# Kernel tuning notes

Measured on AMD Instinct MI355X. Metric: run time of the kernel, lower is better.

The kernel has to match this reference:

```python
import jax, jax.numpy as jnp
import numpy as np

H, O, E, V = 128, 128, 512, 34
B, T, L = 64, 2048, 256


def _lstm(x, wih, whh, bih, bhh):
    # x: [T, B, Din] -> outputs [T, B, H]; PyTorch gate order i, f, g, o
    n = whh.shape[1]
    h0 = jnp.zeros((x.shape[1], n), x.dtype)
    b = bih + bhh
    def step(carry, xt):
        h, c = carry
        g = xt @ wih.T + h @ whh.T + b
        i, f, gg, o = jnp.split(g, 4, axis=-1)
        c = jax.nn.sigmoid(f) * c + jax.nn.sigmoid(i) * jnp.tanh(gg)
        h = jax.nn.sigmoid(o) * jnp.tanh(c)
        return (h, c), h
    _, ys = jax.lax.scan(step, (h0, h0), x)
    return ys


def _conv1d_s2(x, w, b):
    # x: [B, Cin, T], w: [Cout, Cin, 2], kernel=2 stride=2 valid
    y = jax.lax.conv_general_dilated(x, w, (2,), 'VALID', dimension_numbers=('NCH', 'OIH', 'NCH'))
    return y + b[None, :, None]


def setup_inputs():
    key = jax.random.key(0)
    ctr = [0]
    def mk(shape, s=0.05):
        ctr[0] += 1
        return jax.random.normal(jax.random.fold_in(key, ctr[0]), shape, dtype=jnp.float32) * s
    inp = {}
    inp['utter'] = mk((B, T, 40), 1.0)
    inp['targets'] = jax.random.randint(jax.random.fold_in(key, 999), (B, L), 0, V)
    inp['wih_f'] = mk((4 * H, 40)); inp['whh_f'] = mk((4 * H, H)); inp['bih_f'] = mk((4 * H,)); inp['bhh_f'] = mk((4 * H,))
    inp['wih_r'] = mk((4 * H, 40)); inp['whh_r'] = mk((4 * H, H)); inp['bih_r'] = mk((4 * H,)); inp['bhh_r'] = mk((4 * H,))
    inp['c1w'] = mk((H, 2 * H, 2)); inp['c1b'] = mk((H,))
    inp['wih1'] = mk((4 * H, H)); inp['whh1'] = mk((4 * H, H)); inp['bih1'] = mk((4 * H,)); inp['bhh1'] = mk((4 * H,))
    inp['c2w'] = mk((H, H, 2)); inp['c2b'] = mk((H,))
    inp['wih2'] = mk((4 * H, H)); inp['whh2'] = mk((4 * H, H)); inp['bih2'] = mk((4 * H,)); inp['bhh2'] = mk((4 * H,))
    inp['kw'] = mk((O, H)); inp['kb'] = mk((O,)); inp['vw'] = mk((O, H)); inp['vb'] = mk((O,))
    inp['wihd'] = mk((4 * O, O + E)); inp['whhd'] = mk((4 * O, O)); inp['bihd'] = mk((4 * O,)); inp['bhhd'] = mk((4 * O,))
    inp['w1'] = mk((V, O)); inp['b1'] = mk((V,)); inp['w2'] = mk((V, O)); inp['b2'] = mk((V,))
    inp['w3'] = mk((V, V)); inp['b3'] = mk((V,))
    inp['emb'] = mk((V, E), 1.0)
    inp['sh0'] = mk((B, O)); inp['sc0'] = mk((B, O))
    return inp


def _forward(utter, targets, wih_f, whh_f, bih_f, bhh_f, wih_r, whh_r, bih_r, bhh_r,
             c1w, c1b, wih1, whh1, bih1, bhh1, c2w, c2b, wih2, whh2, bih2, bhh2,
             kw, kb, vw, vb, wihd, whhd, bihd, bhhd, w1, b1, w2, b2, w3, b3,
             emb, sh0, sc0):
    # ---- Listener (encoder) ----
    x = jnp.transpose(utter, (1, 0, 2))            # [T, B, 40]
    fwd = _lstm(x, wih_f, whh_f, bih_f, bhh_f)
    bwd = _lstm(x[::-1], wih_r, whh_r, bih_r, bhh_r)[::-1]
    h = jnp.concatenate([fwd, bwd], axis=-1)       # [T, B, 2H]
    h = jnp.transpose(h, (1, 2, 0))                # [B, 2H, T]
    h = _conv1d_s2(h, c1w, c1b)                    # [B, H, T/2]
    h = jnp.transpose(h, (2, 0, 1))                # [T/2, B, H]
    h = _lstm(h, wih1, whh1, bih1, bhh1)
    h = jnp.transpose(h, (1, 2, 0))
    h = _conv1d_s2(h, c2w, c2b)                    # [B, H, T/4]
    h = jnp.transpose(h, (2, 0, 1))
    h = _lstm(h, wih2, whh2, bih2, bhh2)
    h = jnp.transpose(h, (1, 0, 2))                # [B, T/4, H]
    hk = h @ kw.T + kb                              # [B, T/4, O]
    hv = h @ vw.T + vb
    # ---- Speller (decoder) ----
    ys = jnp.transpose(emb[targets], (1, 0, 2))[:-1]   # [L-1, B, E]
    mask = jnp.ones((utter.shape[0], hk.shape[1]), utter.dtype)  # all full-length
    bd = bihd + bhhd
    def step(carry, y_in):
        c, sh, sc = carry
        g = jnp.concatenate([y_in, c], axis=1) @ wihd.T + sh @ whhd.T + bd
        i, f, gg, o = jnp.split(g, 4, axis=-1)
        sc_n = jax.nn.sigmoid(f) * sc + jax.nn.sigmoid(i) * jnp.tanh(gg)
        sh_n = jax.nn.sigmoid(o) * jnp.tanh(sc_n)
        # NOTE: original attends with the cell state sc (faithful to source)
        att = jax.nn.softmax(jnp.einsum('btd,bd->bt', hk, sc_n), axis=1) * mask
        att = att / jnp.sum(att, axis=1, keepdims=True)
        c_n = jnp.einsum('bt,btd->bd', att, hv)
        out = jax.nn.relu(sh_n @ w1.T + b1 + c_n @ w2.T + b2)
        out = jax.nn.softmax(out @ w3.T + b3, axis=1)
        return (c_n, sh_n, sc_n), out
    c0 = jnp.zeros_like(sh0)
    _, preds = jax.lax.scan(step, (c0, sh0, sc0), ys)
    return jnp.transpose(preds, (1, 0, 2))         # [B, L-1, V]


def reference(utter, targets, wih_f, whh_f, bih_f, bhh_f, wih_r, whh_r, bih_r, bhh_r,
              c1w, c1b, wih1, whh1, bih1, bhh1, c2w, c2b, wih2, whh2, bih2, bhh2,
              kw, kb, vw, vb, wihd, whhd, bihd, bhhd, w1, b1, w2, b2, w3, b3,
              emb, sh0, sc0):
    return _forward(utter, targets, wih_f, whh_f, bih_f, bhh_f, wih_r, whh_r, bih_r, bhh_r,
                    c1w, c1b, wih1, whh1, bih1, bhh1, c2w, c2b, wih2, whh2, bih2, bhh2,
                    kw, kb, vw, vb, wihd, whhd, bihd, bhhd, w1, b1, w2, b2, w3, b3,
                    emb, sh0, sc0)
```

## Files before the change

### kernel.cpp

```cpp
#include <hip/hip_runtime.h>

typedef _Float16 half_t;
typedef _Float16 __attribute__((ext_vector_type(2))) half2_t;

__device__ __forceinline__ float fdot2_(half2_t a, half2_t b, float c) {
#if __has_builtin(__builtin_amdgcn_fdot2)
    return __builtin_amdgcn_fdot2(a, b, c, false);
#else
    return c + (float)a[0] * (float)b[0] + (float)a[1] * (float)b[1];
#endif
}
__device__ __forceinline__ half2_t h2(float a, float b) {
    half2_t r; r[0] = (half_t)a; r[1] = (half_t)b; return r;
}
__device__ __forceinline__ half2_t bc2(unsigned int u) {
    return __builtin_bit_cast(half2_t, u);
}
__device__ __forceinline__ unsigned int pk2(float a, float b) {
    return __builtin_bit_cast(unsigned int, h2(a, b));
}
__device__ __forceinline__ float sigm(float x) { return 1.0f / (1.0f + __expf(-x)); }
__device__ __forceinline__ float tanh_(float x) { return 1.0f - 2.0f / (1.0f + __expf(2.0f * x)); }
__device__ __forceinline__ unsigned int packbf2(float a, float b) {
    unsigned int ua = __float_as_uint(a);
    ua = (ua + 0x7fffu + ((ua >> 16) & 1u)) >> 16;
    unsigned int ub = __float_as_uint(b);
    ub = (ub + 0x7fffu + ((ub >> 16) & 1u)) >> 16;
    return ua | (ub << 16);
}
__device__ __forceinline__ float blo(unsigned int u) { return __uint_as_float(u << 16); }
__device__ __forceinline__ float bhi(unsigned int u) { return __uint_as_float(u & 0xffff0000u); }

__global__ __launch_bounds__(256) void packw_k(
    const float* __restrict__ src, unsigned int* __restrict__ dst, int cols, int nq)
{
    int g = blockIdx.x * 256 + threadIdx.x;
    if (g >= 512 * nq * 4) return;
    int k = g & 3, t = g >> 2;
    int tid = t & 511, q = t >> 9;
    int r = (tid & 3) * 128 + (tid >> 2);
    int col = (q * 4 + k) * 2;
    dst[g] = pk2(src[(size_t)r * cols + col], src[(size_t)r * cols + col + 1]);
}

__global__ __launch_bounds__(512, 1) void lstm1_k(
    const float* __restrict__ utter,
    const unsigned int* __restrict__ Whf, const unsigned int* __restrict__ Whr,
    const unsigned int* __restrict__ Wxf, const unsigned int* __restrict__ Wxr,
    const float* __restrict__ bih_f, const float* __restrict__ bhh_f,
    const float* __restrict__ bih_r, const float* __restrict__ bhh_r,
    unsigned short* __restrict__ Hf, unsigned short* __restrict__ Hr,
    const int* __restrict__ targets, const float* __restrict__ emb,
    const float* __restrict__ wihd, const float* __restrict__ bihd,
    const float* __restrict__ bhhd, float* __restrict__ Yp)
{
    __shared__ __align__(16) union {
        struct { half_t h_h[2][128]; half_t x2[2][8][48]; float ring[8][128]; } l;
        struct { float As[2][16][68]; float Ws[2][16][68]; } g;
    } sm;
    const int tid = threadIdx.x;

    if (blockIdx.x >= 128) {
        const int half = tid >> 8, ht = tid & 255;
        float (*As)[68] = sm.g.As[half];
        float (*Ws)[68] = sm.g.Ws[half];
        const int kk = ht & 15, mm = ht >> 4;
        const int tm = ht & 15, tn = ht >> 4;
        const int base = (blockIdx.x - 128) * 2 + half;
        for (int it = 0; it < 16; ++it) {
            int tile = base + it * 128;
            bool active = tile < 2040;
            int t2 = active ? tile : 0;
            int n0 = (t2 & 7) * 64, m0 = (t2 >> 3) * 64;
            const float* arow[4];
#pragma unroll
            for (int r = 0; r < 4; ++r) {
                int m = m0 + mm + 16 * r;
                int l = m >> 6, bb = m & 63;
                arow[r] = emb + (size_t)targets[bb * 256 + l] * 512;
            }
            float acc[4][4];
#pragma unroll
            for (int i = 0; i < 4; ++i)
#pragma unroll
                for (int jj = 0; jj < 4; ++jj) acc[i][jj] = 0.0f;
            for (int k0 = 0; k0 < 512; k0 += 16) {
#pragma unroll
                for (int r = 0; r < 4; ++r) {
                    As[kk][mm + 16 * r] = arow[r][k0 + kk];
                    Ws[kk][mm + 16 * r] = wihd[(size_t)(n0 + mm + 16 * r) * 640 + k0 + kk];
                }
                __syncthreads();
#pragma unroll
                for (int q = 0; q < 16; ++q) {
                    float4 a = reinterpret_cast<const float4*>(&As[q][0])[tm];
                    float4 w = reinterpret_cast<const float4*>(&Ws[q][0])[tn];
                    acc[0][0] += a.x * w.x; acc[0][1] += a.x * w.y; acc[0][2] += a.x * w.z; acc[0][3] += a.x * w.w;
                    acc[1][0] += a.y * w.x; acc[1][1] += a.y * w.y; acc[1][2] += a.y * w.z; acc[1][3] += a.y * w.w;
                    acc[2][0] += a.z * w.x; acc[2][1] += a.z * w.y; acc[2][2] += a.z * w.z; acc[2][3] += a.z * w.w;
                    acc[3][0] += a.w * w.x; acc[3][1] += a.w * w.y; acc[3][2] += a.w * w.z; acc[3][3] += a.w * w.w;
                }
                __syncthreads();
            }
            if (active) {
#pragma unroll
                for (int i = 0; i < 4; ++i) {
                    int m = m0 + tm * 4 + i;
#pragma unroll
                    for (int jj = 0; jj < 4; ++jj) {
                        int n = n0 + tn * 4 + jj;
                        Yp[(size_t)m * 512 + n] = acc[i][jj] + bihd[n] + bhhd[n];
                    }
                }
            }
        }
        return;
    }

    const int b = blockIdx.x & 63;
    const int dir = blockIdx.x >> 6;
    const unsigned int* Whp = dir ? Whr : Whf;
    const unsigned int* Wxp = dir ? Wxr : Wxf;
    const float* bih = dir ? bih_r : bih_f;
    const float* bhh = dir ? bhh_r : bhh_f;
    unsigned short* Hout = dir ? Hr : Hf;
    const int j = tid >> 2, gate = tid & 3;

    uint4 wh[16];
    {
        const uint4* W4 = reinterpret_cast<const uint4*>(Whp);
#pragma unroll
        for (int q = 0; q < 16; ++q) wh[q] = W4[q * 512 + tid];
    }
    uint4 wx[5];
    {
        const uint4* W4 = reinterpret_cast<const uint4*>(Wxp);
#pragma unroll
        for (int q = 0; q < 5; ++q) wx[q] = W4[q * 512 + tid];
    }
    const int r = gate * 128 + j;
    const float bias = bih[r] + bhh[r];
    float c = 0.0f;
    if (tid < 128) { sm.l.h_h[0][tid] = (half_t)0.0f; }
    const int xs = tid / 40, xc = tid % 40;
    if (tid < 320) {
        int tt0 = dir ? (2047 - xs) : xs;
        sm.l.x2[0][xs][xc] = (half_t)utter[((size_t)b * 2048 + tt0) * 40 + xc];
    }
    __syncthreads();

    for (int tc = 0; tc < 2048; tc += 8) {
        const int ph = (tc >> 3) & 1;
        float xreg = 0.0f;
        if (tid < 320) {
            int tn = tc + 8 + xs; if (tn > 2047) tn = 2047;
            int ttn = dir ? (2047 - tn) : tn;
            xreg = utter[((size_t)b * 2048 + ttn) * 40 + xc];
        }
#pragma unroll
        for (int s = 0; s < 8; ++s) {
            const int hb = (tc + s) & 1;
            float g0 = bias, g1 = 0.f, g2 = 0.f, g3 = 0.f;
            {
                const uint4* x4p = reinterpret_cast<const uint4*>(&sm.l.x2[ph][s][0]);
#pragma unroll
                for (int q = 0; q < 5; ++q) {
                    uint4 u = x4p[q];
                    g0 = fdot2_(bc2(wx[q].x), bc2(u.x), g0);
                    g1 = fdot2_(bc2(wx[q].y), bc2(u.y), g1);
                    g2 = fdot2_(bc2(wx[q].z), bc2(u.z), g2);
                    g3 = fdot2_(bc2(wx[q].w), bc2(u.w), g3);
                }
                const uint4* h4p = reinterpret_cast<const uint4*>(&sm.l.h_h[hb][0]);
#pragma unroll
                for (int q = 0; q < 16; ++q) {
                    uint4 u = h4p[q];
                    g0 = fdot2_(bc2(wh[q].x), bc2(u.x), g0);
                    g1 = fdot2_(bc2(wh[q].y), bc2(u.y), g1);
                    g2 = fdot2_(bc2(wh[q].z), bc2(u.z), g2);
                    g3 = fdot2_(bc2(wh[q].w), bc2(u.w), g3);
                }
            }
            float g = (g0 + g1) + (g2 + g3);
            float act = (gate == 2) ? tanh_(g) : sigm(g);
            float f_ = __shfl_xor(act, 1);
            float gg = __shfl_xor(act, 2);
            float o_ = __shfl_xor(act, 3);
            c = f_ * c + act * gg;
            float hh = o_ * tanh_(c);
            if (gate == 0) {
                sm.l.h_h[hb ^ 1][j] = (half_t)hh;
                sm.l.ring[s][j] = hh;
            }
            if (s == 7 && tid < 320)
                sm.l.x2[ph ^ 1][xs][xc] = (half_t)xreg;
            __syncthreads();
        }
        {
            int s2 = tid >> 6, pr = tid & 63;
            int t = tc + s2;
            int tt = dir ? (2047 - t) : t;
            unsigned int v = pk2(sm.l.ring[s2][2 * pr], sm.l.ring[s2][2 * pr + 1]);
            reinterpret_cast<unsigned int*>(Hout)[((size_t)tt * 64 + b) * 64 + pr] = v;
        }
    }
}

__global__ __launch_bounds__(512, 1) void lstm_k(
    const unsigned short* __restrict__ Ph,
    const unsigned int* __restrict__ Wh,
    void* __restrict__ Hout, int T, int outHalf)
{
    const int tid = threadIdx.x;
    const int b = blockIdx.x;
    const int j = tid >> 2, gate = tid & 3;
    __shared__ __align__(16) half_t h_h[2][128];
    __shared__ __align__(16) float ring[8][128];
    uint4 wh[16];
    {
        const uint4* W4 = reinterpret_cast<const uint4*>(Wh);
#pragma unroll
        for (int q = 0; q < 16; ++q) wh[q] = W4[q * 512 + tid];
    }
    float c = 0.0f;
    if (tid < 128) h_h[0][tid] = (half_t)0.0f;
    const size_t pbase = (size_t)b * T;
    float pcur[8], pnext[8];
#pragma unroll
    for (int s = 0; s < 8; ++s)
        pcur[s] = (float)__builtin_bit_cast(half_t, Ph[(pbase + s) * 512 + tid]);
    __syncthreads();

    for (int tc = 0; tc < T; tc += 8) {
#pragma unroll
        for (int s = 0; s < 8; ++s) {
            int tn = tc + 8 + s; if (tn > T - 1) tn = T - 1;
            pnext[s] = (float)__builtin_bit_cast(half_t, Ph[(pbase + tn) * 512 + tid]);
        }
#pragma unroll
        for (int s = 0; s < 8; ++s) {
            const int hb = (tc + s) & 1;
            float g0 = pcur[s], g1 = 0.f, g2 = 0.f, g3 = 0.f;
            const uint4* h4p = reinterpret_cast<const uint4*>(&h_h[hb][0]);
#pragma unroll
            for (int q = 0; q < 16; ++q) {
                uint4 u = h4p[q];
                g0 = fdot2_(bc2(wh[q].x), bc2(u.x), g0);
                g1 = fdot2_(bc2(wh[q].y), bc2(u.y), g1);
                g2 = fdot2_(bc2(wh[q].z), bc2(u.z), g2);
                g3 = fdot2_(bc2(wh[q].w), bc2(u.w), g3);
            }
            float g = (g0 + g1) + (g2 + g3);
            float act = (gate == 2) ? tanh_(g) : sigm(g);
            float f_ = __shfl_xor(act, 1);
            float gg = __shfl_xor(act, 2);
            float o_ = __shfl_xor(act, 3);
            c = f_ * c + act * gg;
            float hh = o_ * tanh_(c);
            if (gate == 0) {
                h_h[hb ^ 1][j] = (half_t)hh;
                ring[s][j] = hh;
            }
            __syncthreads();
        }
        {
            int s2 = tid >> 6, pr = tid & 63;
            int t = tc + s2;
            if (outHalf) {
                unsigned int v = pk2(ring[s2][2 * pr], ring[s2][2 * pr + 1]);
                reinterpret_cast<unsigned int*>(Hout)[((size_t)t * 64 + b) * 64 + pr] = v;
            } else {
                float2 v = make_float2(ring[s2][2 * pr], ring[s2][2 * pr + 1]);
                *reinterpret_cast<float2*>(
                    &reinterpret_cast<float*>(Hout)[((size_t)t * 64 + b) * 128 + 2 * pr]) = v;
            }
        }
#pragma unroll
        for (int s = 0; s < 8; ++s) pcur[s] = pnext[s];
    }
}

template <int CIN>
__global__ __launch_bounds__(128) void conv_k(
    const unsigned short* __restrict__ HA, const unsigned short* __restrict__ HB,
    const float* __restrict__ W, const float* __restrict__ bias,
    float* __restrict__ out, int Tout)
{
    __shared__ __align__(16) float xin[64 * CIN];
    const int b = blockIdx.x;
    const int t0 = blockIdx.y * 32;
    const int tid = threadIdx.x;
    for (int idx = tid; idx < 64 * CIN; idx += 128) {
        int tl = idx / CIN, ci = idx % CIN;
        int tau = t0 * 2 + tl;
        unsigned short u;
        if constexpr (CIN == 256) {
            u = (ci < 128) ? HA[(size_t)tau * 8192 + b * 128 + ci]
                           : HB[(size_t)tau * 8192 + b * 128 + (ci - 128)];
        } else {
            u = HA[(size_t)tau * 8192 + b * 128 + ci];
        }
        xin[idx] = (float)__builtin_bit_cast(half_t, u);
    }
    __syncthreads();
    const int co = tid;
    float acc[32];
#pragma unroll
    for (int u = 0; u < 32; ++u) acc[u] = 0.0f;
    const float4* Wrow4 = reinterpret_cast<const float4*>(W + (size_t)co * 2 * CIN);
    const float4* xin4 = reinterpret_cast<const float4*>(xin);
    for (int c4 = 0; c4 < CIN / 4; ++c4) {
        float4 wA = Wrow4[2 * c4];
        float4 wB = Wrow4[2 * c4 + 1];
#pragma unroll
        for (int u = 0; u < 32; ++u) {
            float4 x0 = xin4[(2 * u) * (CIN / 4) + c4];
            float4 x1 = xin4[(2 * u + 1) * (CIN / 4) + c4];
            acc[u] += wA.x * x0.x + wA.y * x1.x + wA.z * x0.y + wA.w * x1.y
                    + wB.x * x0.z + wB.y * x1.z + wB.z * x0.w + wB.w * x1.w;
        }
    }
    float bs = bias[co];
#pragma unroll
    for (int u = 0; u < 32; ++u)
        out[((size_t)b * Tout + t0 + u) * 128 + co] = acc[u] + bs;
}

__global__ __launch_bounds__(256) void gemm_k(
    const float* __restrict__ A, const float* __restrict__ W, int ldw,
    const float* __restrict__ bias1, const float* __restrict__ bias2,
    void* __restrict__ C, int M, int N, int K, int mode, int Tdim)
{
    __shared__ __align__(16) float As[16][68];
    __shared__ __align__(16) float Ws[16][68];
    const int tid = threadIdx.x;
    const int m0 = blockIdx.x * 64, n0 = blockIdx.y * 64;
    const int kk = tid & 15, mm = tid >> 4;
    const int tm = tid & 15, tn = tid >> 4;
    float acc[4][4];
#pragma unroll
    for (int i = 0; i < 4; ++i)
#pragma unroll
        for (int jj = 0; jj < 4; ++jj) acc[i][jj] = 0.0f;

    for (int k0 = 0; k0 < K; k0 += 16) {
#pragma unroll
        for (int r = 0; r < 4; ++r) {
            As[kk][mm + 16 * r] = A[(size_t)(m0 + mm + 16 * r) * K + k0 + kk];
            Ws[kk][mm + 16 * r] = W[(size_t)(n0 + mm + 16 * r) * ldw + k0 + kk];
        }
        __syncthreads();
#pragma unroll
        for (int q = 0; q < 16; ++q) {
            float4 a = reinterpret_cast<const float4*>(&As[q][0])[tm];
            float4 w = reinterpret_cast<const float4*>(&Ws[q][0])[tn];
            acc[0][0] += a.x * w.x; acc[0][1] += a.x * w.y; acc[0][2] += a.x * w.z; acc[0][3] += a.x * w.w;
            acc[1][0] += a.y * w.x; acc[1][1] += a.y * w.y; acc[1][2] += a.y * w.z; acc[1][3] += a.y * w.w;
            acc[2][0] += a.z * w.x; acc[2][1] += a.z * w.y; acc[2][2] += a.z * w.z; acc[2][3] += a.z * w.w;
            acc[3][0] += a.w * w.x; acc[3][1] += a.w * w.y; acc[3][2] += a.w * w.z; acc[3][3] += a.w * w.w;
        }
        __syncthreads();
    }
    float bv[4];
#pragma unroll
    for (int jj = 0; jj < 4; ++jj) {
        int n = n0 + tn * 4 + jj;
        float v = 0.0f;
        if (bias1) v += bias1[n];
        if (bias2) v += bias2[n];
        bv[jj] = v;
    }
#pragma unroll
    for (int i = 0; i < 4; ++i) {
        int m = m0 + tm * 4 + i;
#pragma unroll
        for (int jj = 0; jj < 4; ++jj) {
            int n = n0 + tn * 4 + jj;
            float v = acc[i][jj] + bv[jj];
            if (mode == 0) {
                ((float*)C)[(size_t)m * N + n] = v;
            } else if (mode == 1) {
                int bb = m & 63, tt = m >> 6;
                ((float*)C)[((size_t)bb * N + n) * Tdim + tt] = v;
            } else if (mode == 2) {
                ((unsigned short*)C)[(size_t)m * N + n] =
                    __builtin_bit_cast(unsigned short, (half_t)v);
            } else {
                ((unsigned short*)C)[(size_t)m * 512 + (n & 127) * 4 + (n >> 7)] =
                    __builtin_bit_cast(unsigned short, (half_t)v);
            }
        }
    }
}

__global__ __launch_bounds__(256) void packq_k(
    const float* __restrict__ src, unsigned int* __restrict__ dst,
    int srcCols, int colOff, int nq, int rows)
{
    int g = blockIdx.x * 256 + threadIdx.x;
    if (g >= rows * nq * 4) return;
    int k = g & 3, t = g >> 2;
    int j = t % rows, q = t / rows;
    int p = q * 4 + k;
    const float* s = src + (size_t)j * srcCols + colOff + 2 * p;
    dst[g] = pk2(s[0], s[1]);
}

__global__ __launch_bounds__(1024) void packhv2_k(
    const float* __restrict__ hvT, unsigned int* __restrict__ hvq)
{
    int b = blockIdx.x;
    for (int it = 0; it < 32; ++it) {
        int idx = it * 1024 + threadIdx.x;
        int tq = idx >> 7, d = idx & 127;
        const float* s = hvT + ((size_t)b * 128 + d) * 512 + 2 * tq;
        hvq[(size_t)b * 32768 + idx] = packbf2(s[0], s[1]);
    }
}

__global__ __launch_bounds__(512, 1) void decoder_k(
    const float* __restrict__ Yp,
    const unsigned int* __restrict__ Wd,
    const float* __restrict__ hk,
    const unsigned int* __restrict__ hvq,
    const float* __restrict__ sh0, const float* __restrict__ sc0,
    float* __restrict__ SHs, float* __restrict__ Cs)
{
    __shared__ unsigned int hk_lds[512][66];
    __shared__ float acts[512];
    __shared__ float pfl[512];
    __shared__ __align__(16) half_t sh_h[128];
    __shared__ __align__(16) float sc_f[128];
    __shared__ __align__(16) half_t c_h[128];
    __shared__ __align__(16) float att[512];
    __shared__ float red[8];
    __shared__ __align__(16) float ringSH[8][128];
    __shared__ __align__(16) float ringC[8][128];

    const int tid = threadIdx.x;
    const int b = blockIdx.x;
    const int gt = tid >> 7;

    uint4 wh[16];
    {
        const uint4* W4 = reinterpret_cast<const uint4*>(Wd);
#pragma unroll
        for (int q = 0; q < 16; ++q) wh[q] = W4[q * 512 + tid];
    }
    const uint4* Wc4 = reinterpret_cast<const uint4*>(Wd) + 8192;

    {
        const float4* hp = reinterpret_cast<const float4*>(hk + ((size_t)tid * 64 + b) * 128);
#pragma unroll
        for (int q = 0; q < 32; ++q) {
            float4 v = hp[q];
            hk_lds[tid][2 * q]     = packbf2(v.x, v.y);
            hk_lds[tid][2 * q + 1] = packbf2(v.z, v.w);
        }
    }
    float sc_r = 0.0f;
    if (tid < 128) {
        sh_h[tid] = (half_t)sh0[b * 128 + tid];
        sc_r = sc0[b * 128 + tid];
        sc_f[tid] = sc_r;
        c_h[tid] = (half_t)0.0f;
    }
    __syncthreads();

    const int wid = tid >> 6, lane = tid & 63;
    const int g4 = tid >> 7, d = tid & 127;
    const unsigned int* hvp = hvq + (size_t)b * 32768 + (size_t)(g4 * 64) * 128 + d;
    const float2* att2 = reinterpret_cast<const float2*>(att);

    for (int lc = 0; lc < 255; lc += 8) {
        const int ns = (255 - lc < 8) ? (255 - lc) : 8;
        float ypv[8];
#pragma unroll
        for (int s = 0; s < 8; ++s) {
            int ll = lc + s; if (ll > 254) ll = 254;
            ypv[s] = Yp[((size_t)ll * 64 + b) * 512 + tid];
        }
        for (int s = 0; s < ns; ++s) {
            {
                float g0 = 0.f, g1 = 0.f, g2 = 0.f, g3 = 0.f;
                const uint4* s4 = reinterpret_cast<const uint4*>(sh_h);
#pragma unroll
                for (int q = 0; q < 16; ++q) {
                    uint4 u = s4[q];
                    g0 = fdot2_(bc2(wh[q].x), bc2(u.x), g0);
                    g1 = fdot2_(bc2(wh[q].y), bc2(u.y), g1);
                    g2 = fdot2_(bc2(wh[q].z), bc2(u.z), g2);
                    g3 = fdot2_(bc2(wh[q].w), bc2(u.w), g3);
                }
                const uint4* c4 = reinterpret_cast<const uint4*>(c_h);
#pragma unroll
                for (int q = 0; q < 16; ++q) {
                    uint4 w = Wc4[q * 512 + tid];
                    uint4 u = c4[q];
                    g0 = fdot2_(bc2(w.x), bc2(u.x), g0);
                    g1 = fdot2_(bc2(w.y), bc2(u.y), g1);
                    g2 = fdot2_(bc2(w.z), bc2(u.z), g2);
                    g3 = fdot2_(bc2(w.w), bc2(u.w), g3);
                }
                float g = (g0 + g1) + (g2 + g3) + ypv[s];
                acts[tid] = (gt == 2) ? tanh_(g) : sigm(g);
            }
            __syncthreads();
            if (tid < 128) {
                float i_ = acts[tid];
                float f_ = acts[128 + tid];
                float g_ = acts[256 + tid];
                float o_ = acts[384 + tid];
                sc_r = f_ * sc_r + i_ * g_;
                float hh = o_ * tanh_(sc_r);
                sh_h[tid] = (half_t)hh;
                sc_f[tid] = sc_r;
                ringSH[s][tid] = hh;
            }
            __syncthreads();
            {
                float e0 = 0.f, e1 = 0.f, e2 = 0.f, e3 = 0.f;
                const uint2* hkr = reinterpret_cast<const uint2*>(&hk_lds[tid][0]);
                const float4* sc4 = reinterpret_cast<const float4*>(sc_f);
#pragma unroll
                for (int q = 0; q < 32; ++q) {
                    uint2 u = hkr[q];
                    float4 sv = sc4[q];
                    e0 += blo(u.x) * sv.x; e1 += bhi(u.x) * sv.y;
                    e2 += blo(u.y) * sv.z; e3 += bhi(u.y) * sv.w;
                }
                float p = __expf((e0 + e1) + (e2 + e3));
                att[tid] = p;
                float ps = p;
#pragma unroll
                for (int off = 32; off; off >>= 1) ps += __shfl_xor(ps, off);
                if (lane == 0) red[wid] = ps;
            }
            __syncthreads();
            {
                float a0 = 0.f, a1 = 0.f;
#pragma unroll 8
                for (int i = 0; i < 64; i += 2) {
                    unsigned int u0 = hvp[(size_t)i * 128];
                    unsigned int u1 = hvp[(size_t)(i + 1) * 128];
                    float2 w0 = att2[g4 * 64 + i];
                    float2 w1 = att2[g4 * 64 + i + 1];
                    a0 += blo(u0) * w0.x + bhi(u0) * w0.y;
                    a1 += blo(u1) * w1.x + bhi(u1) * w1.y;
                }
                pfl[tid] = a0 + a1;
            }
            __syncthreads();
            if (tid < 128) {
                float S = ((red[0] + red[1]) + (red[2] + red[3]))
                        + ((red[4] + red[5]) + (red[6] + red[7]));
                float cv = (pfl[tid] + pfl[128 + tid] + pfl[256 + tid] + pfl[384 + tid]) / S;
                c_h[tid] = (half_t)cv;
                ringC[s][tid] = cv;
            }
            __syncthreads();
        }
        for (int idx = tid; idx < ns * 128; idx += 512) {
            int s2 = idx >> 7, dd = idx & 127;
            SHs[((size_t)(lc + s2) * 64 + b) * 128 + dd] = ringSH[s2][dd];
            Cs[((size_t)(lc + s2) * 64 + b) * 128 + dd] = ringC[s2][dd];
        }
    }
}

__global__ __launch_bounds__(256) void mlp_k(
    const float* __restrict__ SHs, const float* __restrict__ Cs,
    const float* __restrict__ w1, const float* __restrict__ b1,
    const float* __restrict__ w2, const float* __restrict__ b2,
    const float* __restrict__ w3, const float* __restrict__ b3,
    float* __restrict__ out)
{
    __shared__ float o_l[4][34];
    const int sub = threadIdx.x >> 6, lane = threadIdx.x & 63;
    const int m = blockIdx.x * 4 + sub;
    const int l = m >> 6, b = m & 63;
    if (lane < 34) {
        float o1 = b1[lane] + b2[lane];
        const float4* w1r = reinterpret_cast<const float4*>(w1 + lane * 128);
        const float4* w2r = reinterpret_cast<const float4*>(w2 + lane * 128);
        const float4* sh4 = reinterpret_cast<const float4*>(SHs + (size_t)m * 128);
        const float4* c4  = reinterpret_cast<const float4*>(Cs + (size_t)m * 128);
#pragma unroll 8
        for (int q = 0; q < 32; ++q) {
            float4 a = w1r[q], h = sh4[q], w = w2r[q], cc = c4[q];
            o1 += a.x * h.x + a.y * h.y + a.z * h.z + a.w * h.w
                + w.x * cc.x + w.y * cc.y + w.z * cc.z + w.w * cc.w;
        }
        o_l[sub][lane] = fmaxf(o1, 0.0f);
    }
    __syncthreads();
    if (lane < 34) {
        float zz = b3[lane];
        const float* w3r = w3 + lane * 34;
        for (int v = 0; v < 34; ++v) zz += w3r[v] * o_l[sub][v];
        __syncthreads();
        o_l[sub][lane] = zz;
        __syncthreads();
        float zm = o_l[sub][0];
        for (int v = 1; v < 34; ++v) zm = fmaxf(zm, o_l[sub][v]);
        float Ssum = 0.0f;
        for (int v = 0; v < 34; ++v) Ssum += __expf(o_l[sub][v] - zm);
        out[((size_t)b * 255 + l) * 34 + lane] = __expf(zz - zm) / Ssum;
    }
}

extern "C" void kernel_launch(void* const* d_in, const int* in_sizes, int n_in,
                              void* d_out, int out_size, void* d_ws, size_t ws_size,
                              hipStream_t stream) {
    (void)in_sizes; (void)n_in; (void)out_size; (void)ws_size;
    const float* utter = (const float*)d_in[0];
    const int*   targets = (const int*)d_in[1];
    const float* wih_f = (const float*)d_in[2];
    const float* whh_f = (const float*)d_in[3];
    const float* bih_f = (const float*)d_in[4];
    const float* bhh_f = (const float*)d_in[5];
    const float* wih_r = (const float*)d_in[6];
    const float* whh_r = (const float*)d_in[7];
    const float* bih_r = (const float*)d_in[8];
    const float* bhh_r = (const float*)d_in[9];
    const float* c1w = (const float*)d_in[10];
    const float* c1b = (const float*)d_in[11];
    const float* wih1 = (const float*)d_in[12];
    const float* whh1 = (const float*)d_in[13];
    const float* bih1 = (const float*)d_in[14];
    const float* bhh1 = (const float*)d_in[15];
    const float* c2w = (const float*)d_in[16];
    const float* c2b = (const float*)d_in[17];
    const float* wih2 = (const float*)d_in[18];
    const float* whh2 = (const float*)d_in[19];
    const float* bih2 = (const float*)d_in[20];
    const float* bhh2 = (const float*)d_in[21];
    const float* kw = (const float*)d_in[22];
    const float* kb = (const float*)d_in[23];
    const float* vw = (const float*)d_in[24];
    const float* vb = (const float*)d_in[25];
    const float* wihd = (const float*)d_in[26];
    const float* whhd = (const float*)d_in[27];
    const float* bihd = (const float*)d_in[28];
    const float* bhhd = (const float*)d_in[29];
    const float* w1 = (const float*)d_in[30];
    const float* b1 = (const float*)d_in[31];
    const float* w2 = (const float*)d_in[32];
    const float* b2 = (const float*)d_in[33];
    const float* w3 = (const float*)d_in[34];
    const float* b3 = (const float*)d_in[35];
    const float* emb = (const float*)d_in[36];
    const float* sh0 = (const float*)d_in[37];
    const float* sc0 = (const float*)d_in[38];

    char* ws = (char*)d_ws;
    const size_t MB = 1ull << 20;
    unsigned int* W = (unsigned int*)(ws + 0);
    unsigned int* Wd   = W + 0;
    unsigned int* Wl1f = W + 65536;
    unsigned int* Wl1r = W + 98304;
    unsigned int* Wl2  = W + 131072;
    unsigned int* Wl3  = W + 163840;
    unsigned int* Wxf  = W + 196608;
    unsigned int* Wxr  = W + 206848;

    unsigned short* Hf_h   = (unsigned short*)(ws + 1 * MB);
    unsigned short* Hr_h   = (unsigned short*)(ws + 33 * MB);
    float*          Yp     = (float*)(ws + 65 * MB);
    float*          conv1o = (float*)(ws + 97 * MB);
    unsigned short* P2_h   = (unsigned short*)(ws + 1 * MB);
    unsigned short* H2_h   = (unsigned short*)(ws + 97 * MB);
    float*          conv2o = (float*)(ws + 113 * MB);
    unsigned short* P3_h   = (unsigned short*)(ws + 1 * MB);
    float*          H3     = (float*)(ws + 33 * MB);
    float*          hkb    = (float*)(ws + 49 * MB);
    float*          hvT    = (float*)(ws + 97 * MB);
    unsigned int*   hvq    = (unsigned int*)(ws + 113 * MB);
    float*          SHsave = (float*)(ws + 121 * MB);
    float*          Csave  = (float*)(ws + 130 * MB);

    packq_k<<<128, 256, 0, stream>>>(whhd, Wd + 0,     128, 0,   16, 512);
    packq_k<<<128, 256, 0, stream>>>(wihd, Wd + 32768, 640, 512, 16, 512);
    packw_k<<<128, 256, 0, stream>>>(whh_f, Wl1f, 128, 16);
    packw_k<<<128, 256, 0, stream>>>(whh_r, Wl1r, 128, 16);
    packw_k<<<128, 256, 0, stream>>>(whh1, Wl2, 128, 16);
    packw_k<<<128, 256, 0, stream>>>(whh2, Wl3, 128, 16);
    packw_k<<<40, 256, 0, stream>>>(wih_f, Wxf, 40, 5);
    packw_k<<<40, 256, 0, stream>>>(wih_r, Wxr, 40, 5);

    lstm1_k<<<192, 512, 0, stream>>>(utter, Wl1f, Wl1r, Wxf, Wxr,
                                     bih_f, bhh_f, bih_r, bhh_r, Hf_h, Hr_h,
                                     targets, emb, wihd, bihd, bhhd, Yp);
    conv_k<256><<<dim3(64, 32), 128, 0, stream>>>(Hf_h, Hr_h, c1w, c1b, conv1o, 1024);
    gemm_k<<<dim3(1024, 8), 256, 0, stream>>>(conv1o, wih1, 128, bih1, bhh1,
                                              P2_h, 65536, 512, 128, 3, 0);
    lstm_k<<<64, 512, 0, stream>>>(P2_h, Wl2, H2_h, 1024, 1);
    conv_k<128><<<dim3(64, 16), 128, 0, stream>>>(H2_h, nullptr, c2w, c2b, conv2o, 512);
    gemm_k<<<dim3(512, 8), 256, 0, stream>>>(conv2o, wih2, 128, bih2, bhh2,
                                             P3_h, 32768, 512, 128, 3, 0);
    lstm_k<<<64, 512, 0, stream>>>(P3_h, Wl3, H3, 512, 0);
    gemm_k<<<dim3(512, 2), 256, 0, stream>>>(H3, kw, 128, kb, nullptr,
                                             hkb, 32768, 128, 128, 0, 0);
    gemm_k<<<dim3(512, 2), 256, 0, stream>>>(H3, vw, 128, vb, nullptr,
                                             hvT, 32768, 128, 128, 1, 512);
    packhv2_k<<<64, 1024, 0, stream>>>(hvT, hvq);
    decoder_k<<<64, 512, 0, stream>>>(Yp, Wd, hkb, hvq, sh0, sc0, SHsave, Csave);
    mlp_k<<<4080, 256, 0, stream>>>(SHsave, Csave, w1, b1, w2, b2, w3, b3, (float*)d_out);
}
```

Before: 5.181 ms.

## Replace shuffle-based gate exchange in lstm_k with shared-memory gates and extra barrier

The lstm_k kernel for layers 2 and 3 now gives each thread one full gate row (thread = gate*128 + unit). It loads raw fp32 whh rows and packs them to half in registers, so the packed-weight kernels and the interleaved GEMM output mode are no longer needed. Gate activations go through shared memory, and only 128 threads update c and h. This adds a second __syncthreads per timestep and leaves 3/4 of the threads idle during the cell update, while dropping the cross-lane shuffles and the double-buffered h. Per-thread reads of a 512-byte weight row are strided across lanes, so the one-time weight load is less coalesced.

```diff
diff --git a/kernel.cpp b/kernel.cpp
--- a/kernel.cpp
+++ b/kernel.cpp
@@ -208,58 +208,65 @@
 
 __global__ __launch_bounds__(512, 1) void lstm_k(
     const unsigned short* __restrict__ Ph,
-    const unsigned int* __restrict__ Wh,
+    const float* __restrict__ whh,
     void* __restrict__ Hout, int T, int outHalf)
 {
     const int tid = threadIdx.x;
     const int b = blockIdx.x;
-    const int j = tid >> 2, gate = tid & 3;
-    __shared__ __align__(16) half_t h_h[2][128];
+    const int j = tid;
+    const int gt = tid >> 7;
+    __shared__ float acts[512];
+    __shared__ __align__(16) half_t h_h[128];
     __shared__ __align__(16) float ring[8][128];
-    uint4 wh[16];
+    unsigned int wr2[64];
     {
-        const uint4* W4 = reinterpret_cast<const uint4*>(Wh);
-#pragma unroll
-        for (int q = 0; q < 16; ++q) wh[q] = W4[q * 512 + tid];
+        const float4* wp = reinterpret_cast<const float4*>(whh + j * 128);
+#pragma unroll
+        for (int m = 0; m < 32; ++m) {
+            float4 v = wp[m];
+            wr2[2 * m]     = pk2(v.x, v.y);
+            wr2[2 * m + 1] = pk2(v.z, v.w);
+        }
     }
     float c = 0.0f;
-    if (tid < 128) h_h[0][tid] = (half_t)0.0f;
+    if (tid < 128) h_h[tid] = (half_t)0.0f;
     const size_t pbase = (size_t)b * T;
     float pcur[8], pnext[8];
 #pragma unroll
     for (int s = 0; s < 8; ++s)
-        pcur[s] = (float)__builtin_bit_cast(half_t, Ph[(pbase + s) * 512 + tid]);
+        pcur[s] = (float)__builtin_bit_cast(half_t, Ph[(pbase + s) * 512 + j]);
     __syncthreads();
 
     for (int tc = 0; tc < T; tc += 8) {
 #pragma unroll
         for (int s = 0; s < 8; ++s) {
             int tn = tc + 8 + s; if (tn > T - 1) tn = T - 1;
-            pnext[s] = (float)__builtin_bit_cast(half_t, Ph[(pbase + tn) * 512 + tid]);
+            pnext[s] = (float)__builtin_bit_cast(half_t, Ph[(pbase + tn) * 512 + j]);
         }
 #pragma unroll
         for (int s = 0; s < 8; ++s) {
-            const int hb = (tc + s) & 1;
             float g0 = pcur[s], g1 = 0.f, g2 = 0.f, g3 = 0.f;
-            const uint4* h4p = reinterpret_cast<const uint4*>(&h_h[hb][0]);
+            const uint4* h4p = reinterpret_cast<const uint4*>(h_h);
 #pragma unroll
             for (int q = 0; q < 16; ++q) {
                 uint4 u = h4p[q];
-                g0 = fdot2_(bc2(wh[q].x), bc2(u.x), g0);
-                g1 = fdot2_(bc2(wh[q].y), bc2(u.y), g1);
-                g2 = fdot2_(bc2(wh[q].z), bc2(u.z), g2);
-                g3 = fdot2_(bc2(wh[q].w), bc2(u.w), g3);
+                g0 = fdot2_(bc2(wr2[4 * q]),     bc2(u.x), g0);
+                g1 = fdot2_(bc2(wr2[4 * q + 1]), bc2(u.y), g1);
+                g2 = fdot2_(bc2(wr2[4 * q + 2]), bc2(u.z), g2);
+                g3 = fdot2_(bc2(wr2[4 * q + 3]), bc2(u.w), g3);
             }
             float g = (g0 + g1) + (g2 + g3);
-            float act = (gate == 2) ? tanh_(g) : sigm(g);
-            float f_ = __shfl_xor(act, 1);
-            float gg = __shfl_xor(act, 2);
-            float o_ = __shfl_xor(act, 3);
-            c = f_ * c + act * gg;
-            float hh = o_ * tanh_(c);
-            if (gate == 0) {
-                h_h[hb ^ 1][j] = (half_t)hh;
-                ring[s][j] = hh;
+            acts[j] = (gt == 2) ? tanh_(g) : sigm(g);
+            __syncthreads();
+            if (tid < 128) {
+                float i_ = acts[tid];
+                float f_ = acts[128 + tid];
+                float g_ = acts[256 + tid];
+                float o_ = acts[384 + tid];
+                c = f_ * c + i_ * g_;
+                float hh = o_ * tanh_(c);
+                h_h[tid] = (half_t)hh;
+                ring[s][tid] = hh;
             }
             __syncthreads();
         }
@@ -382,11 +389,8 @@
             } else if (mode == 1) {
                 int bb = m & 63, tt = m >> 6;
                 ((float*)C)[((size_t)bb * N + n) * Tdim + tt] = v;
-            } else if (mode == 2) {
+            } else {
                 ((unsigned short*)C)[(size_t)m * N + n] =
-                    __builtin_bit_cast(unsigned short, (half_t)v);
-            } else {
-                ((unsigned short*)C)[(size_t)m * 512 + (n & 127) * 4 + (n >> 7)] =
                     __builtin_bit_cast(unsigned short, (half_t)v);
             }
         }
@@ -659,10 +663,8 @@
     unsigned int* Wd   = W + 0;
     unsigned int* Wl1f = W + 65536;
     unsigned int* Wl1r = W + 98304;
-    unsigned int* Wl2  = W + 131072;
-    unsigned int* Wl3  = W + 163840;
-    unsigned int* Wxf  = W + 196608;
-    unsigned int* Wxr  = W + 206848;
+    unsigned int* Wxf  = W + 131072;
+    unsigned int* Wxr  = W + 141312;
 
     unsigned short* Hf_h   = (unsigned short*)(ws + 1 * MB);
     unsigned short* Hr_h   = (unsigned short*)(ws + 33 * MB);
@@ -683,8 +685,6 @@
     packq_k<<<128, 256, 0, stream>>>(wihd, Wd + 32768, 640, 512, 16, 512);
     packw_k<<<128, 256, 0, stream>>>(whh_f, Wl1f, 128, 16);
     packw_k<<<128, 256, 0, stream>>>(whh_r, Wl1r, 128, 16);
-    packw_k<<<128, 256, 0, stream>>>(whh1, Wl2, 128, 16);
-    packw_k<<<128, 256, 0, stream>>>(whh2, Wl3, 128, 16);
     packw_k<<<40, 256, 0, stream>>>(wih_f, Wxf, 40, 5);
     packw_k<<<40, 256, 0, stream>>>(wih_r, Wxr, 40, 5);
 
@@ -693,12 +693,12 @@
                                      targets, emb, wihd, bihd, bhhd, Yp);
     conv_k<256><<<dim3(64, 32), 128, 0, stream>>>(Hf_h, Hr_h, c1w, c1b, conv1o, 1024);
     gemm_k<<<dim3(1024, 8), 256, 0, stream>>>(conv1o, wih1, 128, bih1, bhh1,
-                                              P2_h, 65536, 512, 128, 3, 0);
-    lstm_k<<<64, 512, 0, stream>>>(P2_h, Wl2, H2_h, 1024, 1);
+                                              P2_h, 65536, 512, 128, 2, 0);
+    lstm_k<<<64, 512, 0, stream>>>(P2_h, whh1, H2_h, 1024, 1);
     conv_k<128><<<dim3(64, 16), 128, 0, stream>>>(H2_h, nullptr, c2w, c2b, conv2o, 512);
     gemm_k<<<dim3(512, 8), 256, 0, stream>>>(conv2o, wih2, 128, bih2, bhh2,
-                                             P3_h, 32768, 512, 128, 3, 0);
-    lstm_k<<<64, 512, 0, stream>>>(P3_h, Wl3, H3, 512, 0);
+                                             P3_h, 32768, 512, 128, 2, 0);
+    lstm_k<<<64, 512, 0, stream>>>(P3_h, whh2, H3, 512, 0);
     gemm_k<<<dim3(512, 2), 256, 0, stream>>>(H3, kw, 128, kb, nullptr,
                                              hkb, 32768, 128, 128, 0, 0);
     gemm_k<<<dim3(512, 2), 256, 0, stream>>>(H3, vw, 128, vb, nullptr,
```

Result: no change. 5.176 ms (-0.1%).
